# Kernel tuning notes

Hardware: AMD Instinct MI355X
Metric: run time of the kernel (lower is better)

## Reference

```python
import jax, jax.numpy as jnp
import numpy as np


def _gcn_norm(edge_index, num_nodes):
    """Add self-loops and compute symmetric normalization coeffs (PyG GCNConv default)."""
    loop = jnp.arange(num_nodes, dtype=edge_index.dtype)
    row = jnp.concatenate([edge_index[0], loop])  # source nodes
    col = jnp.concatenate([edge_index[1], loop])  # target nodes
    deg = jax.ops.segment_sum(jnp.ones_like(col, dtype=jnp.float32), col,
                              num_segments=num_nodes)
    dinv = jnp.where(deg > 0, jax.lax.rsqrt(deg), 0.0)
    norm = dinv[row] * dinv[col]  # [E + N]
    return row, col, norm


def _gcn_conv(x, W, b, row, col, norm, num_nodes):
    xw = x @ W                                   # [N, out]
    msg = xw[row] * norm[:, None]                # gather + scale, [E+N, out]
    out = jax.ops.segment_sum(msg, col, num_segments=num_nodes)  # scatter-add
    return out + b


def setup_inputs() -> dict:
    key = jax.random.key(0)
    ks = jax.random.split(key, 12)
    N, E, F, H, C, G = 100000, 1600000, 64, 64, 10, 128
    x = jax.random.normal(ks[0], (N, F), dtype=jnp.float32)
    edge_index = jax.random.randint(ks[1], (2, E), 0, N, dtype=jnp.int64)
    batch = jnp.sort(jax.random.randint(ks[2], (N,), 0, G, dtype=jnp.int64))
    def glorot(k, fan_in, fan_out):
        s = jnp.sqrt(6.0 / (fan_in + fan_out))
        return jax.random.uniform(k, (fan_in, fan_out), jnp.float32, -s, s)
    return {
        "x": x, "edge_index": edge_index, "batch": batch, "num_graphs": G,
        "W0": glorot(ks[3], F, H), "b0": jnp.zeros((H,), jnp.float32),
        "W1": glorot(ks[4], H, H), "b1": jnp.zeros((H,), jnp.float32),
        "W2": glorot(ks[5], H, H), "b2": jnp.zeros((H,), jnp.float32),
        "Wro": glorot(ks[6], H, C), "bro": jnp.zeros((C,), jnp.float32),
    }


def reference(x, edge_index, batch, num_graphs, W0, b0, W1, b1, W2, b2, Wro, bro):
    N = x.shape[0]
    row, col, norm = _gcn_norm(edge_index, N)
    for W, b in ((W0, b0), (W1, b1), (W2, b2)):
        x = jax.nn.silu(_gcn_conv(x, W, b, row, col, norm, N))
        # dropout p=0.0 / eval mode -> identity
    # global_mean_pool over batch ids
    sums = jax.ops.segment_sum(x, batch, num_segments=num_graphs)   # [G, H]
    cnts = jax.ops.segment_sum(jnp.ones((N,), x.dtype), batch, num_segments=num_graphs)
    pooled = sums / jnp.maximum(cnts, 1.0)[:, None]
    # readout: Linear + ReLU (make_mlp with hidden_layers=1), then log_softmax
    logits = jax.nn.relu(pooled @ Wro + bro)
    return jax.nn.log_softmax(logits, axis=1)
```

## Files before the change

### kernel.cpp

```cpp
#include <hip/hip_runtime.h>
#include <hip/hip_fp16.h>


#define CH 256
#define BSH 7
#define BNODES 128

typedef _Float16 half8 __attribute__((ext_vector_type(8)));
typedef float float4v __attribute__((ext_vector_type(4)));

__global__ __launch_bounds__(256) void k_hist(const int* __restrict__ col, int E, int Ec, int NB,
                                              int* __restrict__ histG) {
    __shared__ int h[1024];
    int c = blockIdx.x, tid = threadIdx.x;
    for (int i = tid; i < NB; i += 256) h[i] = 0;
    __syncthreads();
    int lo = c * Ec, hi = min(E, lo + Ec);
    for (int e = lo + tid; e < hi; e += 256) atomicAdd(&h[col[e] >> BSH], 1);
    __syncthreads();
    for (int i = tid; i < NB; i += 256) histG[c * NB + i] = h[i];
}

__global__ void k_scanb(int* __restrict__ histG, int NB, int* __restrict__ btot) {
    int b = blockIdx.x;
    int l = threadIdx.x;
    int v[4], p[4];
#pragma unroll
    for (int k = 0; k < 4; ++k) { v[k] = histG[(k * 64 + l) * NB + b]; p[k] = v[k]; }
    for (int off = 1; off < 64; off <<= 1) {
#pragma unroll
        for (int k = 0; k < 4; ++k) {
            int t = __shfl_up(p[k], off);
            if (l >= off) p[k] += t;
        }
    }
    int acc = 0;
#pragma unroll
    for (int k = 0; k < 4; ++k) {
        int tot = __shfl(p[k], 63);
        histG[(k * 64 + l) * NB + b] = acc + p[k] - v[k];
        acc += tot;
    }
    if (l == 0) btot[b] = acc;
}

__global__ void k_scant(const int* __restrict__ btot, int NB, int E, int* __restrict__ bstart) {
    __shared__ int s[1024];
    int tid = threadIdx.x;
    int v = (tid < NB) ? btot[tid] : 0;
    s[tid] = v;
    __syncthreads();
    for (int off = 1; off < 1024; off <<= 1) {
        int t = (tid >= off) ? s[tid - off] : 0;
        __syncthreads();
        s[tid] += t;
        __syncthreads();
    }
    if (tid < NB) bstart[tid] = s[tid] - v;
    if (tid == 0) bstart[NB] = E;
}

__global__ __launch_bounds__(1024) void k_scatter(const int* __restrict__ col, const int* __restrict__ row,
                                                  int E, int Ec, int NB,
                                                  const int* __restrict__ histG,
                                                  const int* __restrict__ bstart,
                                                  unsigned int* __restrict__ edges) {
    __shared__ int cur[1024];
    int c = blockIdx.x, tid = threadIdx.x;
    for (int i = tid; i < NB; i += 1024) cur[i] = bstart[i] + histG[c * NB + i];
    __syncthreads();
    int lo = c * Ec, hi = min(E, lo + Ec);
    for (int e = lo + tid; e < hi; e += 1024) {
        int cc = col[e];
        int b = cc >> BSH;
        int pos = atomicAdd(&cur[b], 1);
        edges[pos] = (unsigned int)row[e] | ((unsigned int)(cc & (BNODES - 1)) << 25);
    }
}

__global__ __launch_bounds__(512) void k_sort2(const unsigned int* __restrict__ edges,
                                               const int* __restrict__ bstart, int N, int E, int NB,
                                               int* __restrict__ srcs, int* __restrict__ starts,
                                               float* __restrict__ dinv) {
    __shared__ int cnt[BNODES];
    __shared__ int cur[BNODES];
    int b = blockIdx.x, tid = threadIdx.x;
    if (tid < BNODES) cnt[tid] = 0;
    __syncthreads();
    int lo = bstart[b], hi = bstart[b + 1];
    for (int e = lo + tid; e < hi; e += 512) atomicAdd(&cnt[edges[e] >> 25], 1);
    __syncthreads();
    if (tid < 64) {
        int v0 = cnt[tid], v1 = cnt[64 + tid];
        int p0 = v0, p1 = v1;
        for (int off = 1; off < 64; off <<= 1) {
            int t0 = __shfl_up(p0, off);
            int t1 = __shfl_up(p1, off);
            if (tid >= off) { p0 += t0; p1 += t1; }
        }
        int A = __shfl(p0, 63);
        cur[tid] = lo + p0 - v0;
        cur[64 + tid] = lo + A + p1 - v1;
    }
    __syncthreads();
    int ng = b * BNODES + tid;
    if (tid < BNODES && ng < N) {
        starts[ng] = cur[tid];
        dinv[ng] = rsqrtf((float)cnt[tid] + 1.0f);
    }
    if (b == 0 && tid == 0) starts[N] = E;
    __syncthreads();
    for (int e = lo + tid; e < hi; e += 512) {
        unsigned int p = edges[e];
        int pos = atomicAdd(&cur[p >> 25], 1);
        srcs[pos] = (int)((p & 0x1FFFFFFu) << 3);
    }
}

template <int IN_HALF>
__global__ __launch_bounds__(256) void k_gemm(const void* __restrict__ xin,
                                              const float* __restrict__ W,
                                              const float* __restrict__ dinv,
                                              __half* __restrict__ yh, int N) {
    __shared__ float sW[64 * 64];
    int tid = threadIdx.x;
    for (int k = tid; k < 4096; k += 256) sW[k] = W[k];
    __syncthreads();
    int lane = tid & 63, wv = tid >> 6;
    int c16 = lane & 15, kg = lane >> 4;
    half8 bf[4][2];
#pragma unroll
    for (int ct = 0; ct < 4; ++ct)
#pragma unroll
        for (int ks = 0; ks < 2; ++ks)
#pragma unroll
            for (int j = 0; j < 8; ++j)
                bf[ct][ks][j] = (_Float16)sW[(ks * 32 + kg * 8 + j) * 64 + ct * 16 + c16];

    int tiles = (N + 15) >> 4;
    for (int t = blockIdx.x * 4 + wv; t < tiles; t += gridDim.x * 4) {
        int base = t << 4;
        int arow = base + c16;
        half8 af0, af1;
        if (arow < N) {
            if (IN_HALF) {
                const __half* xh = (const __half*)xin;
                af0 = *(const half8*)(xh + (size_t)arow * 64 + kg * 8);
                af1 = *(const half8*)(xh + (size_t)arow * 64 + 32 + kg * 8);
            } else {
                const float* xf = (const float*)xin;
                float4 u0 = *(const float4*)(xf + (size_t)arow * 64 + kg * 8);
                float4 u1 = *(const float4*)(xf + (size_t)arow * 64 + kg * 8 + 4);
                float4 u2 = *(const float4*)(xf + (size_t)arow * 64 + 32 + kg * 8);
                float4 u3 = *(const float4*)(xf + (size_t)arow * 64 + 32 + kg * 8 + 4);
                af0[0]=(_Float16)u0.x; af0[1]=(_Float16)u0.y; af0[2]=(_Float16)u0.z; af0[3]=(_Float16)u0.w;
                af0[4]=(_Float16)u1.x; af0[5]=(_Float16)u1.y; af0[6]=(_Float16)u1.z; af0[7]=(_Float16)u1.w;
                af1[0]=(_Float16)u2.x; af1[1]=(_Float16)u2.y; af1[2]=(_Float16)u2.z; af1[3]=(_Float16)u2.w;
                af1[4]=(_Float16)u3.x; af1[5]=(_Float16)u3.y; af1[6]=(_Float16)u3.z; af1[7]=(_Float16)u3.w;
            }
        } else {
#pragma unroll
            for (int j = 0; j < 8; ++j) { af0[j] = (_Float16)0.f; af1[j] = (_Float16)0.f; }
        }
#pragma unroll
        for (int ct = 0; ct < 4; ++ct) {
            float4v c = {0.f, 0.f, 0.f, 0.f};
            c = __builtin_amdgcn_mfma_f32_16x16x32_f16(af0, bf[ct][0], c, 0, 0, 0);
            c = __builtin_amdgcn_mfma_f32_16x16x32_f16(af1, bf[ct][1], c, 0, 0, 0);
#pragma unroll
            for (int q = 0; q < 4; ++q) {
                int rr = base + kg * 4 + q;
                if (rr < N) yh[(size_t)rr * 64 + ct * 16 + c16] = __float2half_rn(c[q] * dinv[rr]);
            }
        }
    }
}

__global__ __launch_bounds__(256) void k_agg(const int* __restrict__ starts,
                                             const int* __restrict__ srcs,
                                             const __half* __restrict__ yh,
                                             const float* __restrict__ dinv,
                                             const float* __restrict__ b,
                                             __half* __restrict__ xh, int N) {
    int wv = (blockIdx.x * blockDim.x + threadIdx.x) >> 6;
    int lane = threadIdx.x & 63;
    int g = lane >> 3, i = lane & 7;
    int node = wv * 8 + g;
    bool valid = node < N;
    const float4* y4 = (const float4*)yh;
    __half2 a0, a1, a2, a3;
    a0 = a1 = a2 = a3 = __half2half2(__ushort_as_half((unsigned short)0));
    int s = 0, t = 0;
    if (valid) {
        s = starts[node]; t = starts[node + 1];
        float4 raw = y4[(size_t)node * 8 + i];
        const __half2* h = (const __half2*)&raw;
        a0 = h[0]; a1 = h[1]; a2 = h[2]; a3 = h[3];
    }
    int e = s;
    for (; e + 3 < t; e += 4) {
        int s0 = srcs[e], s1 = srcs[e + 1], s2 = srcs[e + 2], s3 = srcs[e + 3];
        float4 r0 = y4[(size_t)s0 + i];
        float4 r1 = y4[(size_t)s1 + i];
        float4 r2 = y4[(size_t)s2 + i];
        float4 r3 = y4[(size_t)s3 + i];
        const __half2* h0 = (const __half2*)&r0;
        const __half2* h1 = (const __half2*)&r1;
        const __half2* h2 = (const __half2*)&r2;
        const __half2* h3 = (const __half2*)&r3;
        a0 = __hadd2(__hadd2(__hadd2(a0, h0[0]), h1[0]), __hadd2(h2[0], h3[0]));
        a1 = __hadd2(__hadd2(__hadd2(a1, h0[1]), h1[1]), __hadd2(h2[1], h3[1]));
        a2 = __hadd2(__hadd2(__hadd2(a2, h0[2]), h1[2]), __hadd2(h2[2], h3[2]));
        a3 = __hadd2(__hadd2(__hadd2(a3, h0[3]), h1[3]), __hadd2(h2[3], h3[3]));
    }
    for (; e < t; ++e) {
        int s0 = srcs[e];
        float4 r0 = y4[(size_t)s0 + i];
        const __half2* h0 = (const __half2*)&r0;
        a0 = __hadd2(a0, h0[0]); a1 = __hadd2(a1, h0[1]);
        a2 = __hadd2(a2, h0[2]); a3 = __hadd2(a3, h0[3]);
    }
    if (valid) {
        float d = dinv[node];
        float4 b0 = ((const float4*)b)[2 * i];
        float4 b1 = ((const float4*)b)[2 * i + 1];
        float bb[8] = {b0.x, b0.y, b0.z, b0.w, b1.x, b1.y, b1.z, b1.w};
        float2 f0 = __half22float2(a0), f1 = __half22float2(a1);
        float2 f2 = __half22float2(a2), f3 = __half22float2(a3);
        float sums[8] = {f0.x, f0.y, f1.x, f1.y, f2.x, f2.y, f3.x, f3.y};
        float o[8];
#pragma unroll
        for (int f = 0; f < 8; ++f) {
            float v = d * sums[f] + bb[f];
            o[f] = v / (1.f + __expf(-v));
        }
        float4 outv;
        __half2* oh = (__half2*)&outv;
#pragma unroll
        for (int p = 0; p < 4; ++p) oh[p] = __float22half2_rn(make_float2(o[2 * p], o[2 * p + 1]));
        ((float4*)xh)[(size_t)node * 8 + i] = outv;
    }
}

__global__ void k_pool_readout(const __half2* __restrict__ xh2, const int* __restrict__ batch, int N,
                               const float* __restrict__ Wro, const float* __restrict__ bro,
                               float* __restrict__ out, int C) {
    int g = blockIdx.x;
    int tid = threadIdx.x, wave = tid >> 6, lane = tid & 63;
    int grp = lane >> 5, i = lane & 31;
    __shared__ float part[4][64];
    __shared__ float pooled[64];
    __shared__ float logits[32];
    int lo = 0, hb = N;
    while (lo < hb) { int m = (lo + hb) >> 1; if (batch[m] < g) lo = m + 1; else hb = m; }
    int lo2 = lo, hi2 = N;
    while (lo2 < hi2) { int m = (lo2 + hi2) >> 1; if (batch[m] < g + 1) lo2 = m + 1; else hi2 = m; }
    int hi = lo2;
    float ax = 0.f, ay = 0.f;
    for (int r = lo + wave * 2 + grp; r < hi; r += 8) {
        float2 v = __half22float2(xh2[(size_t)r * 32 + i]);
        ax += v.x; ay += v.y;
    }
    ax += __shfl_xor(ax, 32);
    ay += __shfl_xor(ay, 32);
    if (grp == 0) { part[wave][2 * i] = ax; part[wave][2 * i + 1] = ay; }
    __syncthreads();
    if (tid < 64) {
        float cntf = fmaxf((float)(hi - lo), 1.0f);
        pooled[tid] = (part[0][tid] + part[1][tid] + part[2][tid] + part[3][tid]) / cntf;
    }
    __syncthreads();
    if (tid < C) {
        float a = bro[tid];
        for (int k = 0; k < 64; ++k) a += pooled[k] * Wro[k * C + tid];
        logits[tid] = fmaxf(a, 0.f);
    }
    __syncthreads();
    if (tid == 0) {
        float m = -1e30f;
        for (int c = 0; c < C; ++c) m = fmaxf(m, logits[c]);
        float sum = 0.f;
        for (int c = 0; c < C; ++c) sum += __expf(logits[c] - m);
        float lse = m + __logf(sum);
        for (int c = 0; c < C; ++c) out[g * C + c] = logits[c] - lse;
    }
}

static inline size_t align256(size_t v) { return (v + 255) & ~(size_t)255; }

extern "C" void kernel_launch(void* const* d_in, const int* in_sizes, int n_in,
                              void* d_out, int out_size, void* d_ws, size_t ws_size,
                              hipStream_t stream) {
    const float* x    = (const float*)d_in[0];
    const int*   ei   = (const int*)d_in[1];
    const int*   batch= (const int*)d_in[2];
    const float* W[3] = {(const float*)d_in[4], (const float*)d_in[6], (const float*)d_in[8]};
    const float* b[3] = {(const float*)d_in[5], (const float*)d_in[7], (const float*)d_in[9]};
    const float* Wro  = (const float*)d_in[10];
    const float* bro  = (const float*)d_in[11];

    int N = in_sizes[2];
    int E = in_sizes[1] / 2;
    int C = in_sizes[10] / 64;
    int G = out_size / C;

    const int* row = ei;
    const int* col = ei + E;

    int NB = (N + BNODES - 1) >> BSH;
    int Ec = (E + CH - 1) / CH;

    char* ws = (char*)d_ws;
    size_t off = 0;
    float* dinv    = (float*)(ws + off);        off = align256(off + (size_t)N * 4);
    int*   histG   = (int*)(ws + off);          off = align256(off + (size_t)CH * NB * 4);
    int*   btot    = (int*)(ws + off);          off = align256(off + (size_t)NB * 4);
    int*   bstart  = (int*)(ws + off);          off = align256(off + (size_t)(NB + 1) * 4);
    unsigned int* edges = (unsigned int*)(ws + off); off = align256(off + (size_t)E * 4);
    int*   srcs    = (int*)(ws + off);          off = align256(off + (size_t)E * 4);
    int*   starts  = (int*)(ws + off);          off = align256(off + (size_t)(N + 1) * 4);
    __half* yh     = (__half*)(ws + off);       off = align256(off + (size_t)N * 64 * 2);
    __half* xh     = (__half*)(ws + off);       off = align256(off + (size_t)N * 64 * 2);

    k_hist<<<CH, 256, 0, stream>>>(col, E, Ec, NB, histG);
    k_scanb<<<NB, 64, 0, stream>>>(histG, NB, btot);
    k_scant<<<1, 1024, 0, stream>>>(btot, NB, E, bstart);
    k_scatter<<<CH, 1024, 0, stream>>>(col, row, E, Ec, NB, histG, bstart, edges);
    k_sort2<<<NB, 512, 0, stream>>>(edges, bstart, N, E, NB, srcs, starts, dinv);

    int aggB = (N + 31) / 32;
    int gemmB = 1568;

    k_gemm<0><<<gemmB, 256, 0, stream>>>(x, W[0], dinv, yh, N);
    k_agg<<<aggB, 256, 0, stream>>>(starts, srcs, yh, dinv, b[0], xh, N);
    k_gemm<1><<<gemmB, 256, 0, stream>>>(xh, W[1], dinv, yh, N);
    k_agg<<<aggB, 256, 0, stream>>>(starts, srcs, yh, dinv, b[1], xh, N);
    k_gemm<1><<<gemmB, 256, 0, stream>>>(xh, W[2], dinv, yh, N);
    k_agg<<<aggB, 256, 0, stream>>>(starts, srcs, yh, dinv, b[2], xh, N);

    k_pool_readout<<<G, 256, 0, stream>>>((const __half2*)xh, batch, N, Wro, bro, (float*)d_out, C);
}
```

Baseline: 226.4 us.

## Split pooling into chunked atomic partial sums and separate readout; unroll gather by 8

Graph mean-pooling previously ran one 256-thread block per graph (128 blocks) reading roughly 780 nodes each, which underuses the GPU. It now splits nodes into 4096 contiguous chunks, each wave summing its chunk per graph and flushing with atomics into a zeroed float buffer, followed by a small readout kernel. The aggregation loop also gains an 8-wide unrolled gather so more loads are in flight, at the cost of more registers and a different fp16 summation order. It adds a memset and an extra launch.

```diff
diff --git a/kernel.cpp b/kernel.cpp
--- a/kernel.cpp
+++ b/kernel.cpp
@@ -198,24 +198,30 @@
         a0 = h[0]; a1 = h[1]; a2 = h[2]; a3 = h[3];
     }
     int e = s;
+    for (; e + 7 < t; e += 8) {
+        float4 r[8];
+#pragma unroll
+        for (int k = 0; k < 8; ++k) r[k] = y4[(size_t)srcs[e + k] + i];
+#pragma unroll
+        for (int k = 0; k < 8; ++k) {
+            const __half2* h = (const __half2*)&r[k];
+            a0 = __hadd2(a0, h[0]); a1 = __hadd2(a1, h[1]);
+            a2 = __hadd2(a2, h[2]); a3 = __hadd2(a3, h[3]);
+        }
+    }
     for (; e + 3 < t; e += 4) {
-        int s0 = srcs[e], s1 = srcs[e + 1], s2 = srcs[e + 2], s3 = srcs[e + 3];
-        float4 r0 = y4[(size_t)s0 + i];
-        float4 r1 = y4[(size_t)s1 + i];
-        float4 r2 = y4[(size_t)s2 + i];
-        float4 r3 = y4[(size_t)s3 + i];
-        const __half2* h0 = (const __half2*)&r0;
-        const __half2* h1 = (const __half2*)&r1;
-        const __half2* h2 = (const __half2*)&r2;
-        const __half2* h3 = (const __half2*)&r3;
-        a0 = __hadd2(__hadd2(__hadd2(a0, h0[0]), h1[0]), __hadd2(h2[0], h3[0]));
-        a1 = __hadd2(__hadd2(__hadd2(a1, h0[1]), h1[1]), __hadd2(h2[1], h3[1]));
-        a2 = __hadd2(__hadd2(__hadd2(a2, h0[2]), h1[2]), __hadd2(h2[2], h3[2]));
-        a3 = __hadd2(__hadd2(__hadd2(a3, h0[3]), h1[3]), __hadd2(h2[3], h3[3]));
+        float4 r[4];
+#pragma unroll
+        for (int k = 0; k < 4; ++k) r[k] = y4[(size_t)srcs[e + k] + i];
+#pragma unroll
+        for (int k = 0; k < 4; ++k) {
+            const __half2* h = (const __half2*)&r[k];
+            a0 = __hadd2(a0, h[0]); a1 = __hadd2(a1, h[1]);
+            a2 = __hadd2(a2, h[2]); a3 = __hadd2(a3, h[3]);
+        }
     }
     for (; e < t; ++e) {
-        int s0 = srcs[e];
-        float4 r0 = y4[(size_t)s0 + i];
+        float4 r0 = y4[(size_t)srcs[e] + i];
         const __half2* h0 = (const __half2*)&r0;
         a0 = __hadd2(a0, h0[0]); a1 = __hadd2(a1, h0[1]);
         a2 = __hadd2(a2, h0[2]); a3 = __hadd2(a3, h0[3]);
@@ -242,47 +248,55 @@
     }
 }
 
-__global__ void k_pool_readout(const __half2* __restrict__ xh2, const int* __restrict__ batch, int N,
-                               const float* __restrict__ Wro, const float* __restrict__ bro,
-                               float* __restrict__ out, int C) {
+__global__ __launch_bounds__(256) void k_pool1(const __half* __restrict__ xh,
+                                               const int* __restrict__ batch, int N, int chunk,
+                                               float* __restrict__ sums) {
+    int wvg = blockIdx.x * 4 + (threadIdx.x >> 6);
+    int lane = threadIdx.x & 63;
+    int lo = wvg * chunk;
+    int hi = min(N, lo + chunk);
+    if (lo >= hi) return;
+    float acc = 0.f;
+    int gcur = batch[lo];
+    for (int n = lo; n < hi; ++n) {
+        int gn = batch[n];
+        if (gn != gcur) {
+            atomicAdd(&sums[gcur * 64 + lane], acc);
+            acc = 0.f;
+            gcur = gn;
+        }
+        acc += __half2float(xh[(size_t)n * 64 + lane]);
+    }
+    atomicAdd(&sums[gcur * 64 + lane], acc);
+}
+
+__global__ void k_readout(const float* __restrict__ sums, const int* __restrict__ batch, int N,
+                          const float* __restrict__ Wro, const float* __restrict__ bro,
+                          float* __restrict__ out, int C) {
     int g = blockIdx.x;
-    int tid = threadIdx.x, wave = tid >> 6, lane = tid & 63;
-    int grp = lane >> 5, i = lane & 31;
-    __shared__ float part[4][64];
-    __shared__ float pooled[64];
-    __shared__ float logits[32];
+    int j = threadIdx.x;
+    __shared__ float sp[64];
+    __shared__ float sl[32];
     int lo = 0, hb = N;
     while (lo < hb) { int m = (lo + hb) >> 1; if (batch[m] < g) lo = m + 1; else hb = m; }
     int lo2 = lo, hi2 = N;
     while (lo2 < hi2) { int m = (lo2 + hi2) >> 1; if (batch[m] < g + 1) lo2 = m + 1; else hi2 = m; }
-    int hi = lo2;
-    float ax = 0.f, ay = 0.f;
-    for (int r = lo + wave * 2 + grp; r < hi; r += 8) {
-        float2 v = __half22float2(xh2[(size_t)r * 32 + i]);
-        ax += v.x; ay += v.y;
-    }
-    ax += __shfl_xor(ax, 32);
-    ay += __shfl_xor(ay, 32);
-    if (grp == 0) { part[wave][2 * i] = ax; part[wave][2 * i + 1] = ay; }
-    __syncthreads();
-    if (tid < 64) {
-        float cntf = fmaxf((float)(hi - lo), 1.0f);
-        pooled[tid] = (part[0][tid] + part[1][tid] + part[2][tid] + part[3][tid]) / cntf;
-    }
-    __syncthreads();
-    if (tid < C) {
-        float a = bro[tid];
-        for (int k = 0; k < 64; ++k) a += pooled[k] * Wro[k * C + tid];
-        logits[tid] = fmaxf(a, 0.f);
-    }
-    __syncthreads();
-    if (tid == 0) {
+    float cnt = fmaxf((float)(hi2 - lo), 1.0f);
+    sp[j] = sums[g * 64 + j] / cnt;
+    __syncthreads();
+    if (j < C) {
+        float a = bro[j];
+        for (int k = 0; k < 64; ++k) a += sp[k] * Wro[k * C + j];
+        sl[j] = fmaxf(a, 0.f);
+    }
+    __syncthreads();
+    if (j == 0) {
         float m = -1e30f;
-        for (int c = 0; c < C; ++c) m = fmaxf(m, logits[c]);
+        for (int c = 0; c < C; ++c) m = fmaxf(m, sl[c]);
         float sum = 0.f;
-        for (int c = 0; c < C; ++c) sum += __expf(logits[c] - m);
+        for (int c = 0; c < C; ++c) sum += __expf(sl[c] - m);
         float lse = m + __logf(sum);
-        for (int c = 0; c < C; ++c) out[g * C + c] = logits[c] - lse;
+        for (int c = 0; c < C; ++c) out[g * C + c] = sl[c] - lse;
     }
 }
 
@@ -321,6 +335,7 @@
     int*   starts  = (int*)(ws + off);          off = align256(off + (size_t)(N + 1) * 4);
     __half* yh     = (__half*)(ws + off);       off = align256(off + (size_t)N * 64 * 2);
     __half* xh     = (__half*)(ws + off);       off = align256(off + (size_t)N * 64 * 2);
+    float* sums    = (float*)(ws + off);        off = align256(off + (size_t)G * 64 * 4);
 
     k_hist<<<CH, 256, 0, stream>>>(col, E, Ec, NB, histG);
     k_scanb<<<NB, 64, 0, stream>>>(histG, NB, btot);
@@ -338,5 +353,9 @@
     k_gemm<1><<<gemmB, 256, 0, stream>>>(xh, W[2], dinv, yh, N);
     k_agg<<<aggB, 256, 0, stream>>>(starts, srcs, yh, dinv, b[2], xh, N);
 
-    k_pool_readout<<<G, 256, 0, stream>>>((const __half2*)xh, batch, N, Wro, bro, (float*)d_out, C);
-}
+    hipMemsetAsync(sums, 0, (size_t)G * 64 * sizeof(float), stream);
+    int nwaves = 4096;
+    int chunk = (N + nwaves - 1) / nwaves;
+    k_pool1<<<nwaves / 4, 256, 0, stream>>>(xh, batch, N, chunk, sums);
+    k_readout<<<G, 64, 0, stream>>>(sums, batch, N, Wro, bro, (float*)d_out, C);
+}
```

Result: faster. 206.7 us (-8.7%).
